# Kernel optimization log

Measured on AMD Instinct MI355X. Metric: run time of the kernel, lower is better.

Reference implementation:

```python
import jax, jax.numpy as jnp
import numpy as np
import math

B, F, HOP, SR = 64, 4096, 64, 16000


def setup_inputs() -> dict:
    key = jax.random.key(0)
    k1, k2 = jax.random.split(key)
    frequency = jax.random.uniform(k1, (B, F), dtype=jnp.float32) * 1000.0 + 20.0  # Hz
    phase_mod = jax.random.normal(k2, (B, F * HOP), dtype=jnp.float32) * 0.1
    return {"frequency": frequency, "phase_mod": phase_mod, "length": HOP, "sample_rate": SR}


def reference(frequency, phase_mod, length, sample_rate):
    # upsample control-rate frequency to audio rate: [B, F] -> [B, F*length]
    inst_freq = jnp.repeat(frequency, length, axis=-1)
    # phase accumulator
    phase = jnp.cumsum(inst_freq, axis=-1)
    phase = phase - phase[..., :1]
    phase = (2.0 * math.pi) * phase / sample_rate
    phase = phase + phase_mod
    # concrete generate(): sine oscillator
    return jnp.sin(phase)
```

## Files before the change

kernel.cpp:

```cpp
#include <hip/hip_runtime.h>
#include <math.h>


#define BB   64
#define FF   4096
#define NPER (FF * 64)

__device__ inline void hs16(float* x) {
#pragma unroll
    for (int s = 1; s < 16; s <<= 1) {
#pragma unroll
        for (int c = 15; c >= 0; --c) {
            if (c >= s) x[c] = x[c] + x[c - s];
        }
    }
}

__global__ __launch_bounds__(256)
void prescan_kernel(const float* __restrict__ freq, float* __restrict__ scan1g) {
    __shared__ float fr[4096];
    __shared__ float v2[1024];
    __shared__ float v3[64];
    __shared__ float scan3[64];
    __shared__ float scan2[1024];

    const int b = blockIdx.x, tid = threadIdx.x;
    const float* row = freq + b * FF;
    for (int i = tid; i < FF; i += 256) fr[i] = row[i];
    __syncthreads();

    for (int J = tid; J < 1024; J += 256) {
        float x[16];
#pragma unroll
        for (int c = 0; c < 16; ++c) x[c] = 16.0f * fr[4 * J + (c >> 2)];
        hs16(x);
        v2[J] = x[15];
    }
    __syncthreads();

    for (int K = tid; K < 64; K += 256) {
        float x[16];
#pragma unroll
        for (int c = 0; c < 16; ++c) x[c] = v2[16 * K + c];
        hs16(x);
        v3[K] = x[15];
    }
    __syncthreads();

    if (tid == 0) {
        float inner3[64], v4[4];
        for (int M = 0; M < 4; ++M) {
            float x[16];
#pragma unroll
            for (int c = 0; c < 16; ++c) x[c] = v3[16 * M + c];
            hs16(x);
            for (int c = 0; c < 16; ++c) inner3[16 * M + c] = x[c];
            v4[M] = x[15];
        }
        float s4[4];
        s4[0] = v4[0];
        s4[1] = s4[0] + v4[1];
        s4[2] = s4[1] + v4[2];
        s4[3] = s4[2] + v4[3];
        for (int K = 0; K < 64; ++K) {
            const int M = K >> 4;
            const float e4 = (M == 0) ? 0.0f : s4[M - 1];
            scan3[K] = inner3[K] + e4;
        }
    }
    __syncthreads();

    for (int K = tid; K < 64; K += 256) {
        float x[16];
#pragma unroll
        for (int c = 0; c < 16; ++c) x[c] = v2[16 * K + c];
        hs16(x);
        const float e3 = (K == 0) ? 0.0f : scan3[K - 1];
        for (int c = 0; c < 16; ++c) scan2[16 * K + c] = x[c] + e3;
    }
    __syncthreads();

    float* srow = scan1g + b * 16384;
    for (int J = tid; J < 1024; J += 256) {
        float x[16];
#pragma unroll
        for (int c = 0; c < 16; ++c) x[c] = 16.0f * fr[4 * J + (c >> 2)];
        hs16(x);
        const float e2 = (J == 0) ? 0.0f : scan2[J - 1];
        for (int c = 0; c < 16; ++c) srow[16 * J + c] = x[c] + e2;
    }
}

__global__ __launch_bounds__(256)
void osc_kernel(const float* __restrict__ freq,
                const float* __restrict__ pm,
                const float* __restrict__ scan1g,
                float* __restrict__ out) {
    const int i4  = blockIdx.x * blockDim.x + threadIdx.x;
    const int e   = i4 << 2;
    const int b   = e >> 18;
    const int rem = e & (NPER - 1);
    const int f   = rem >> 6;
    const int c0  = rem & 15;
    const int j   = rem >> 4;

    const float fr = freq[b * FF + f];
    const float f0 = freq[b * FF];
    const float excl1 = (j == 0) ? 0.0f : scan1g[b * 16384 + j - 1];

    const float t1 = fr;
    const float t2 = fr + fr;
    const float t3 = t2 + t1;
    const float t4 = t2 + t2;
    const float t5 = t4 + t1;
    const float t6 = t4 + t2;
    const float t7 = t4 + t3;
    const float t8 = t4 + t4;
    const float low[8] = {t1, t2, t3, t4, t5, t6, t7, t8};

    const float4 p4 = ((const float4*)pm)[i4];
    const float pj[4] = {p4.x, p4.y, p4.z, p4.w};
    const float TWOPI_F = 6.28318530717958647692f;

    float oj[4];
#pragma unroll
    for (int k = 0; k < 4; ++k) {
        const int c = c0 + k;
        float inner0;
        if (c < 8)        inner0 = low[c];
        else if (c == 15) inner0 = t8 + t8;
        else              inner0 = t8 + low[c - 8];
        const float ph = inner0 + excl1;
        const float d  = ph - f0;
        const float t  = d * TWOPI_F;
        const float u  = t / 16000.0f;
        const float x  = u + pj[k];
        oj[k] = sinf(x);
    }
    float4 o;
    o.x = oj[0]; o.y = oj[1]; o.z = oj[2]; o.w = oj[3];
    ((float4*)out)[i4] = o;
}

extern "C" void kernel_launch(void* const* d_in, const int* in_sizes, int n_in,
                              void* d_out, int out_size, void* d_ws, size_t ws_size,
                              hipStream_t stream) {
    const float* freq = (const float*)d_in[0];
    const float* pm   = (const float*)d_in[1];
    float* outp   = (float*)d_out;
    float* scan1g = (float*)d_ws;

    prescan_kernel<<<dim3(BB), dim3(256), 0, stream>>>(freq, scan1g);

    const int total4 = (BB * NPER) / 4;
    osc_kernel<<<dim3(total4 / 256), dim3(256), 0, stream>>>(freq, pm, scan1g, outp);
}
```

Measured before the change: 133.7 us.

## Process 16 samples per thread in oscillator and parallelize prescan top level

```diff
diff --git a/kernel.cpp b/kernel.cpp
--- a/kernel.cpp
+++ b/kernel.cpp
@@ -21,6 +21,9 @@
     __shared__ float fr[4096];
     __shared__ float v2[1024];
     __shared__ float v3[64];
+    __shared__ float inner3s[64];
+    __shared__ float v4s[4];
+    __shared__ float s4s[4];
     __shared__ float scan3[64];
     __shared__ float scan2[1024];
 
@@ -47,26 +50,30 @@
     }
     __syncthreads();
 
+    if (tid < 4) {
+        const int M = tid;
+        float x[16];
+#pragma unroll
+        for (int c = 0; c < 16; ++c) x[c] = v3[16 * M + c];
+        hs16(x);
+#pragma unroll
+        for (int c = 0; c < 16; ++c) inner3s[16 * M + c] = x[c];
+        v4s[M] = x[15];
+    }
+    __syncthreads();
+
     if (tid == 0) {
-        float inner3[64], v4[4];
-        for (int M = 0; M < 4; ++M) {
-            float x[16];
-#pragma unroll
-            for (int c = 0; c < 16; ++c) x[c] = v3[16 * M + c];
-            hs16(x);
-            for (int c = 0; c < 16; ++c) inner3[16 * M + c] = x[c];
-            v4[M] = x[15];
-        }
-        float s4[4];
-        s4[0] = v4[0];
-        s4[1] = s4[0] + v4[1];
-        s4[2] = s4[1] + v4[2];
-        s4[3] = s4[2] + v4[3];
-        for (int K = 0; K < 64; ++K) {
-            const int M = K >> 4;
-            const float e4 = (M == 0) ? 0.0f : s4[M - 1];
-            scan3[K] = inner3[K] + e4;
-        }
+        s4s[0] = v4s[0];
+        s4s[1] = s4s[0] + v4s[1];
+        s4s[2] = s4s[1] + v4s[2];
+        s4s[3] = s4s[2] + v4s[3];
+    }
+    __syncthreads();
+
+    for (int K = tid; K < 64; K += 256) {
+        const int M = K >> 4;
+        const float e4 = (M == 0) ? 0.0f : s4s[M - 1];
+        scan3[K] = inner3s[K] + e4;
     }
     __syncthreads();
 
@@ -96,17 +103,14 @@
                 const float* __restrict__ pm,
                 const float* __restrict__ scan1g,
                 float* __restrict__ out) {
-    const int i4  = blockIdx.x * blockDim.x + threadIdx.x;
-    const int e   = i4 << 2;
-    const int b   = e >> 18;
-    const int rem = e & (NPER - 1);
-    const int f   = rem >> 6;
-    const int c0  = rem & 15;
-    const int j   = rem >> 4;
+    const int ib   = blockIdx.x * blockDim.x + threadIdx.x;
+    const int b    = ib >> 14;
+    const int jrow = ib & 16383;
+    const int f    = jrow >> 2;
 
     const float fr = freq[b * FF + f];
     const float f0 = freq[b * FF];
-    const float excl1 = (j == 0) ? 0.0f : scan1g[b * 16384 + j - 1];
+    const float excl1 = (jrow == 0) ? 0.0f : scan1g[b * 16384 + jrow - 1];
 
     const float t1 = fr;
     const float t2 = fr + fr;
@@ -116,30 +120,33 @@
     const float t6 = t4 + t2;
     const float t7 = t4 + t3;
     const float t8 = t4 + t4;
-    const float low[8] = {t1, t2, t3, t4, t5, t6, t7, t8};
+    const float inn[16] = {t1, t2, t3, t4, t5, t6, t7, t8,
+                           t8 + t1, t8 + t2, t8 + t3, t8 + t4,
+                           t8 + t5, t8 + t6, t8 + t7, t8 + t8};
 
-    const float4 p4 = ((const float4*)pm)[i4];
-    const float pj[4] = {p4.x, p4.y, p4.z, p4.w};
+    const float4* pmv  = (const float4*)pm + (size_t)ib * 4;
+    float4*       outv = (float4*)out + (size_t)ib * 4;
     const float TWOPI_F = 6.28318530717958647692f;
 
-    float oj[4];
 #pragma unroll
-    for (int k = 0; k < 4; ++k) {
-        const int c = c0 + k;
-        float inner0;
-        if (c < 8)        inner0 = low[c];
-        else if (c == 15) inner0 = t8 + t8;
-        else              inner0 = t8 + low[c - 8];
-        const float ph = inner0 + excl1;
-        const float d  = ph - f0;
-        const float t  = d * TWOPI_F;
-        const float u  = t / 16000.0f;
-        const float x  = u + pj[k];
-        oj[k] = sinf(x);
+    for (int g = 0; g < 4; ++g) {
+        const float4 p4 = pmv[g];
+        const float pj[4] = {p4.x, p4.y, p4.z, p4.w};
+        float oj[4];
+#pragma unroll
+        for (int k = 0; k < 4; ++k) {
+            const int c = 4 * g + k;
+            const float ph = inn[c] + excl1;
+            const float d  = ph - f0;
+            const float t  = d * TWOPI_F;
+            const float u  = t / 16000.0f;
+            const float x  = u + pj[k];
+            oj[k] = sinf(x);
+        }
+        float4 o;
+        o.x = oj[0]; o.y = oj[1]; o.z = oj[2]; o.w = oj[3];
+        outv[g] = o;
     }
-    float4 o;
-    o.x = oj[0]; o.y = oj[1]; o.z = oj[2]; o.w = oj[3];
-    ((float4*)out)[i4] = o;
 }
 
 extern "C" void kernel_launch(void* const* d_in, const int* in_sizes, int n_in,
@@ -152,6 +159,6 @@
 
     prescan_kernel<<<dim3(BB), dim3(256), 0, stream>>>(freq, scan1g);
 
-    const int total4 = (BB * NPER) / 4;
-    osc_kernel<<<dim3(total4 / 256), dim3(256), 0, stream>>>(freq, pm, scan1g, outp);
+    const int nthreads = (BB * NPER) / 16;
+    osc_kernel<<<dim3(nthreads / 256), dim3(256), 0, stream>>>(freq, pm, scan1g, outp);
 }
```

New measurement: 156.4 us. +17.0%, slower.
